# Kernel tuning notes

Hardware: AMD Instinct MI355X
Metric: run time of the kernel (lower is better)

The kernel has to match this reference:

```python
import jax, jax.numpy as jnp
import numpy as np

N_NODES = 50000

def mpnn_layer(x, edge_index, edge_weight, Wm, Wu, bu):
    # x: [N, Din]; Wm, Wu: [Dout, Din]; bu: [Dout]
    src, dst = edge_index[0], edge_index[1]
    m = x @ Wm.T                                   # [N, Dout] linear message
    msg = edge_weight[:, None] * m[src]            # gather + weight  [E, Dout]
    agg = jax.ops.segment_sum(msg, dst, num_segments=N_NODES)  # scatter-add
    return jnp.tanh(x @ Wu.T + bu + agg)

def setup_inputs() -> dict:
    key = jax.random.key(0)
    ks = jax.random.split(key, 16)
    N, E, D_IN, H, OUT = N_NODES, 800000, 128, 128, 32
    inp = {
        'x': jax.random.normal(ks[0], (N, D_IN), dtype=jnp.float32),
        'edge_index': jax.random.randint(ks[1], (2, E), 0, N, dtype=jnp.int64),
        'edge_weight': jax.random.uniform(ks[2], (E,), dtype=jnp.float32),
    }
    scale = 0.05
    dims = [D_IN, H, H]  # per-layer input dims
    for l in range(3):
        inp[f'Wm{l}'] = jax.random.normal(ks[3 + 3 * l], (H, dims[l]), dtype=jnp.float32) * scale
        inp[f'Wu{l}'] = jax.random.normal(ks[4 + 3 * l], (H, dims[l]), dtype=jnp.float32) * scale
        inp[f'bu{l}'] = jnp.zeros((H,), dtype=jnp.float32)
    inp['Wout'] = jax.random.normal(ks[13], (OUT, H), dtype=jnp.float32) * scale
    inp['bout'] = jnp.zeros((OUT,), dtype=jnp.float32)
    return inp

def reference(x, edge_index, edge_weight, Wm0, Wu0, bu0, Wm1, Wu1, bu1, Wm2, Wu2, bu2, Wout, bout):
    h = x
    for Wm, Wu, bu in ((Wm0, Wu0, bu0), (Wm1, Wu1, bu1), (Wm2, Wu2, bu2)):
        h = mpnn_layer(h, edge_index, edge_weight, Wm, Wu, bu)
    return h @ Wout.T + bout
```

## Files before the change

kernel.cpp:

```cpp
#include <hip/hip_runtime.h>
#include <hip/hip_bf16.h>
#include <cstddef>


typedef __attribute__((ext_vector_type(8))) short short8;
typedef __attribute__((ext_vector_type(4))) float f32x4;
typedef unsigned short ushort_t;
typedef unsigned int uint_t;

#define BSH 8
#define BSZ 256
#define CAPB 6144
#define TSTRIDE 16
#define EPB 2048

__device__ inline ushort_t f2bf(float f) {
    uint_t u = __float_as_uint(f);
    uint_t r = u + 0x7FFFu + ((u >> 16) & 1u);
    return (ushort_t)(r >> 16);
}
__device__ inline float bf_lo(uint_t u) { return __uint_as_float(u << 16); }
__device__ inline float bf_hi(uint_t u) { return __uint_as_float(u & 0xFFFF0000u); }
__device__ inline uint_t packbf(float a, float b) {
    return (uint_t)f2bf(a) | ((uint_t)f2bf(b) << 16);
}

__device__ inline float fast_tanh(float x) {
    float e = __builtin_amdgcn_exp2f(x * 2.8853900817779268f);
    return 1.f - 2.f * __builtin_amdgcn_rcpf(e + 1.f);
}

__device__ inline int get_dst(const int* __restrict__ ei, int e, int E, int f) {
    if (f) return ei[E + e];
    return ((const int2*)ei)[(size_t)E + e].x;
}
__device__ inline int get_src(const int* __restrict__ ei, int e, int E, int f) {
    if (f) return ei[e];
    return ((const int2*)ei)[e].x;
}

struct SetupArgs {
    const float* Wm0; const float* Wu0;
    const float* Wm1; const float* Wu1;
    const float* Wm2; const float* Wu2;
    const float* Wout;
    const float* x; const int* ei;
    ushort_t* wswz;
    ushort_t* woswz;
    ushort_t* xb;
    int* tails;
    int* flag;
    int N, E, TI;
    int ZT, WB, XB;
};
__global__ __launch_bounds__(256) void setup_kernel(SetupArgs a) {
    int bx = blockIdx.x, t = threadIdx.x;
    if (bx < a.ZT) {
        int i = bx * 256 + t;
        if (i < a.TI) a.tails[i] = 0;
        return;
    }
    bx -= a.ZT;
    if (bx == 0) {
        __shared__ int any;
        if (t == 0) any = 0;
        __syncthreads();
        int n = a.E < 2048 ? a.E : 2048;
        for (int i = t; i < n; i += 256)
            if (a.ei[2 * i + 1] != 0) any = 1;
        __syncthreads();
        if (t == 0) a.flag[0] = any;
        return;
    }
    bx -= 1;
    if (bx < a.WB) {
        int i = bx * 256 + t;
        if (i < 3 * 32768) {
            int l = i >> 15, r2 = i & 32767;
            int ct = r2 >> 12, ks = (r2 >> 9) & 7, lane = (r2 >> 3) & 63, j = r2 & 7;
            int col = ct * 16 + (lane & 15);
            int k = ks * 32 + (lane >> 4) * 8 + j;
            const float* Wm = l == 0 ? a.Wm0 : (l == 1 ? a.Wm1 : a.Wm2);
            const float* Wu = l == 0 ? a.Wu0 : (l == 1 ? a.Wu1 : a.Wu2);
            float v = k < 128 ? Wm[col * 128 + k] : Wu[col * 128 + (k - 128)];
            a.wswz[(size_t)l * 32768 + r2] = f2bf(v);
        } else if (i < 3 * 32768 + 4096) {
            int r2 = i - 3 * 32768;
            int ct = r2 >> 11, ks = (r2 >> 9) & 3, lane = (r2 >> 3) & 63, j = r2 & 7;
            int col = ct * 16 + (lane & 15);
            int k = ks * 32 + (lane >> 4) * 8 + j;
            a.woswz[r2] = f2bf(a.Wout[col * 128 + k]);
        }
        return;
    }
    bx -= a.WB;
    {
        int j = bx * 256 + t;
        if (j < a.N * 32) {
            float4 v = *(const float4*)(a.x + (size_t)j * 4);
            uint2 o;
            o.x = packbf(v.x, v.y);
            o.y = packbf(v.z, v.w);
            *(uint2*)(a.xb + (size_t)j * 4) = o;
        }
    }
}

__global__ __launch_bounds__(256) void bin_kernel(
    const int* __restrict__ ei, const float* __restrict__ ew,
    const int* __restrict__ flag, int* __restrict__ tails,
    uint2* __restrict__ staged, int E, int NB) {
    __shared__ uint2 ent[EPB];
    __shared__ int cnt[256], cur[256], runbase[256];
    const int tid = threadIdx.x;
    const int e0 = blockIdx.x * EPB;
    const int nE = (E - e0) < EPB ? (E - e0) : EPB;
    const int f = flag[0];
    cnt[tid] = 0;
    cur[tid] = 0;
    __syncthreads();
    for (int i = tid; i < nE; i += 256) {
        int e = e0 + i;
        int s = get_src(ei, e, E, f);
        int d = get_dst(ei, e, E, f);
        uint2 v;
        v.x = (uint_t)s | ((uint_t)f2bf(ew[e]) << 16);
        v.y = (uint_t)d;
        ent[i] = v;
        atomicAdd(&cnt[d >> BSH], 1);
    }
    __syncthreads();
    if (tid < NB) {
        int c = cnt[tid];
        runbase[tid] = c ? atomicAdd(&tails[tid * TSTRIDE], c) : 0;
    }
    __syncthreads();
    for (int i = tid; i < nE; i += 256) {
        uint2 v = ent[i];
        int d = (int)v.y;
        int b = d >> BSH;
        int lp = atomicAdd(&cur[b], 1);
        int gp = runbase[b] + lp;
        if (gp < CAPB) {
            uint2 o;
            o.x = v.x;
            o.y = (uint_t)(d & (BSZ - 1));
            staged[(size_t)b * CAPB + gp] = o;
        }
    }
}

__global__ __launch_bounds__(256) void place_kernel(
    const uint2* __restrict__ staged, const int* __restrict__ tails,
    int* __restrict__ cursor, uint_t* __restrict__ csr,
    int2* __restrict__ rowdeg, int N) {
    __shared__ int cnt[256], cur[256], excl[256], sm[256];
    __shared__ int baseSh;
    __shared__ uint_t outb[CAPB];
    const int b = blockIdx.x, tid = threadIdx.x;
    const int node0 = b << BSH;
    int tot = tails[b * TSTRIDE];
    tot = tot < CAPB ? tot : CAPB;
    cnt[tid] = 0;
    __syncthreads();
    const uint2* sp = staged + ((size_t)b * CAPB);
    for (int i = tid; i < tot; i += 256) atomicAdd(&cnt[sp[i].y], 1);
    __syncthreads();
    int c0 = cnt[tid];
    sm[tid] = c0;
    __syncthreads();
    for (int o = 1; o < 256; o <<= 1) {
        int v = tid >= o ? sm[tid - o] : 0;
        __syncthreads();
        sm[tid] += v;
        __syncthreads();
    }
    if (tid == 255) baseSh = atomicAdd(cursor, sm[255]);
    excl[tid] = sm[tid] - c0;
    cur[tid] = 0;
    __syncthreads();
    const int base = baseSh;
    for (int i = tid; i < tot; i += 256) {
        uint2 e = sp[i];
        int pos = excl[e.y] + atomicAdd(&cur[e.y], 1);
        outb[pos] = e.x;
    }
    __syncthreads();
    for (int i = tid; i < tot; i += 256) csr[base + i] = outb[i];
    if (node0 + tid < N) {
        int2 be;
        be.x = base + excl[tid];
        be.y = base + excl[tid] + c0;
        rowdeg[node0 + tid] = be;
    }
}

template <int WITH_OUT>
__global__ __launch_bounds__(512) void fused_layer(
    const uint_t* __restrict__ csr, const int2* __restrict__ rowdeg,
    const ushort_t* __restrict__ h, const ushort_t* __restrict__ Wswz,
    const float* __restrict__ bias, ushort_t* __restrict__ Hout,
    const ushort_t* __restrict__ Woswz, const float* __restrict__ bout,
    float* __restrict__ Cout, int N) {
    __shared__ ushort_t Gt[32 * 128];
    __shared__ ushort_t Ht[32 * 128];
    const int tid = threadIdx.x;
    const int lane = tid & 63;
    const int wv = tid >> 6;
    const int R0 = blockIdx.x * 32;
    const int slot = lane >> 3, f8 = lane & 7;

    const int pp = tid * 16;
    const int srow = pp >> 8;
    const int sx = (pp & 255) ^ ((srow & 7) << 4);
    uint4 hst = *(const uint4*)(h + (size_t)(R0 + srow) * 128 + (sx >> 1));

    int2 be[4];
#pragma unroll
    for (int i = 0; i < 4; ++i) {
        int nd = R0 + wv * 4 + i;
        if (nd < N) be[i] = rowdeg[nd];
        else { be[i].x = 0; be[i].y = 0; }
    }
#pragma unroll
    for (int i = 0; i < 4; ++i) {
        const int lr = wv * 4 + i;
        float s[16];
#pragma unroll
        for (int k = 0; k < 16; ++k) s[k] = 0.f;
        int j = be[i].x + slot;
        const int end = be[i].y;
        for (; j + 8 < end; j += 16) {
            uint_t p0 = csr[j];
            uint_t p1 = csr[j + 8];
            float w0 = bf_hi(p0), w1 = bf_hi(p1);
            const ushort_t* r0 = h + (size_t)(p0 & 0xFFFFu) * 128 + f8 * 16;
            const ushort_t* r1 = h + (size_t)(p1 & 0xFFFFu) * 128 + f8 * 16;
            uint4 v0 = *(const uint4*)(r0);
            uint4 v1 = *(const uint4*)(r0 + 8);
            uint4 u0 = *(const uint4*)(r1);
            uint4 u1 = *(const uint4*)(r1 + 8);
            s[0] += w0 * bf_lo(v0.x);  s[1] += w0 * bf_hi(v0.x);
            s[2] += w0 * bf_lo(v0.y);  s[3] += w0 * bf_hi(v0.y);
            s[4] += w0 * bf_lo(v0.z);  s[5] += w0 * bf_hi(v0.z);
            s[6] += w0 * bf_lo(v0.w);  s[7] += w0 * bf_hi(v0.w);
            s[8] += w0 * bf_lo(v1.x);  s[9] += w0 * bf_hi(v1.x);
            s[10] += w0 * bf_lo(v1.y); s[11] += w0 * bf_hi(v1.y);
            s[12] += w0 * bf_lo(v1.z); s[13] += w0 * bf_hi(v1.z);
            s[14] += w0 * bf_lo(v1.w); s[15] += w0 * bf_hi(v1.w);
            s[0] += w1 * bf_lo(u0.x);  s[1] += w1 * bf_hi(u0.x);
            s[2] += w1 * bf_lo(u0.y);  s[3] += w1 * bf_hi(u0.y);
            s[4] += w1 * bf_lo(u0.z);  s[5] += w1 * bf_hi(u0.z);
            s[6] += w1 * bf_lo(u0.w);  s[7] += w1 * bf_hi(u0.w);
            s[8] += w1 * bf_lo(u1.x);  s[9] += w1 * bf_hi(u1.x);
            s[10] += w1 * bf_lo(u1.y); s[11] += w1 * bf_hi(u1.y);
            s[12] += w1 * bf_lo(u1.z); s[13] += w1 * bf_hi(u1.z);
            s[14] += w1 * bf_lo(u1.w); s[15] += w1 * bf_hi(u1.w);
        }
        if (j < end) {
            uint_t p = csr[j];
            float w = bf_hi(p);
            const ushort_t* row = h + (size_t)(p & 0xFFFFu) * 128 + f8 * 16;
            uint4 v0 = *(const uint4*)(row);
            uint4 v1 = *(const uint4*)(row + 8);
            s[0] += w * bf_lo(v0.x);  s[1] += w * bf_hi(v0.x);
            s[2] += w * bf_lo(v0.y);  s[3] += w * bf_hi(v0.y);
            s[4] += w * bf_lo(v0.z);  s[5] += w * bf_hi(v0.z);
            s[6] += w * bf_lo(v0.w);  s[7] += w * bf_hi(v0.w);
            s[8] += w * bf_lo(v1.x);  s[9] += w * bf_hi(v1.x);
            s[10] += w * bf_lo(v1.y); s[11] += w * bf_hi(v1.y);
            s[12] += w * bf_lo(v1.z); s[13] += w * bf_hi(v1.z);
            s[14] += w * bf_lo(v1.w); s[15] += w * bf_hi(v1.w);
        }
#pragma unroll
        for (int k = 0; k < 16; ++k) s[k] += __shfl_xor(s[k], 8, 64);
#pragma unroll
        for (int k = 0; k < 16; ++k) s[k] += __shfl_xor(s[k], 16, 64);
#pragma unroll
        for (int k = 0; k < 16; ++k) s[k] += __shfl_xor(s[k], 32, 64);
        if (slot == 0) {
            uint4 o0, o1;
            o0.x = packbf(s[0], s[1]);   o0.y = packbf(s[2], s[3]);
            o0.z = packbf(s[4], s[5]);   o0.w = packbf(s[6], s[7]);
            o1.x = packbf(s[8], s[9]);   o1.y = packbf(s[10], s[11]);
            o1.z = packbf(s[12], s[13]); o1.w = packbf(s[14], s[15]);
            const int sw = (lr & 7) << 3;
            *(uint4*)(Gt + lr * 128 + ((f8 * 16) ^ sw)) = o0;
            *(uint4*)(Gt + lr * 128 + ((f8 * 16 + 8) ^ sw)) = o1;
        }
    }
    *(uint4*)((char*)Ht + pp) = hst;
    __syncthreads();

    const int gblk = wv & 1, ctp = wv >> 1;
    const int m = lane & 15, kg = lane >> 4;
    const int lrow = gblk * 16 + m;
    const int lsw = (lrow & 7) << 3;
    const int colL = lane & 15, rq = lane >> 4;

    short8 b0[8], b1[8];
#pragma unroll
    for (int ksp = 0; ksp < 8; ++ksp) {
        b0[ksp] = *(const short8*)(Wswz + (((2 * ctp) * 8 + ksp) * 64 + lane) * 8);
        b1[ksp] = *(const short8*)(Wswz + (((2 * ctp + 1) * 8 + ksp) * 64 + lane) * 8);
    }
    const float bv0 = bias[(2 * ctp) * 16 + colL];
    const float bv1 = bias[(2 * ctp + 1) * 16 + colL];

    f32x4 acc0 = (f32x4){0.f, 0.f, 0.f, 0.f};
    f32x4 acc1 = (f32x4){0.f, 0.f, 0.f, 0.f};
#pragma unroll
    for (int ksp = 0; ksp < 8; ++ksp) {
        const ushort_t* tp = (ksp < 4) ? Gt : Ht;
        short8 av = *(const short8*)(tp + lrow * 128 + (((ksp & 3) * 32 + kg * 8) ^ lsw));
        acc0 = __builtin_amdgcn_mfma_f32_16x16x32_bf16(av, b0[ksp], acc0, 0, 0, 0);
        acc1 = __builtin_amdgcn_mfma_f32_16x16x32_bf16(av, b1[ksp], acc1, 0, 0, 0);
    }
    float v0[4], v1[4];
#pragma unroll
    for (int reg = 0; reg < 4; ++reg) {
        v0[reg] = fast_tanh(acc0[reg] + bv0);
        v1[reg] = fast_tanh(acc1[reg] + bv1);
    }

    if (WITH_OUT == 0) {
#pragma unroll
        for (int reg = 0; reg < 4; ++reg) {
            int gr = R0 + gblk * 16 + rq * 4 + reg;
            if (gr < N) {
                Hout[(size_t)gr * 128 + (2 * ctp) * 16 + colL] = f2bf(v0[reg]);
                Hout[(size_t)gr * 128 + (2 * ctp + 1) * 16 + colL] = f2bf(v1[reg]);
            }
        }
    } else {
        __syncthreads();
#pragma unroll
        for (int reg = 0; reg < 4; ++reg) {
            int lr3 = gblk * 16 + rq * 4 + reg;
            int sw3 = (lr3 & 7) << 3;
            Gt[lr3 * 128 + (((2 * ctp) * 16 + colL) ^ sw3)] = f2bf(v0[reg]);
            Gt[lr3 * 128 + (((2 * ctp + 1) * 16 + colL) ^ sw3)] = f2bf(v1[reg]);
        }
        __syncthreads();
        if (wv < 4) {
            const int og = wv & 1, oc = wv >> 1;
            const int orow = og * 16 + m;
            const int osw = (orow & 7) << 3;
            short8 ob[4];
#pragma unroll
            for (int ks = 0; ks < 4; ++ks)
                ob[ks] = *(const short8*)(Woswz + ((oc * 4 + ks) * 64 + lane) * 8);
            f32x4 oacc = (f32x4){0.f, 0.f, 0.f, 0.f};
#pragma unroll
            for (int ks = 0; ks < 4; ++ks) {
                short8 av = *(const short8*)(Gt + orow * 128 + ((ks * 32 + kg * 8) ^ osw));
                oacc = __builtin_amdgcn_mfma_f32_16x16x32_bf16(av, ob[ks], oacc, 0, 0, 0);
            }
            const float obv = bout[oc * 16 + colL];
#pragma unroll
            for (int reg = 0; reg < 4; ++reg) {
                int gr = R0 + og * 16 + rq * 4 + reg;
                if (gr < N) Cout[(size_t)gr * 32 + oc * 16 + colL] = oacc[reg] + obv;
            }
        }
    }
}

extern "C" void kernel_launch(void* const* d_in, const int* in_sizes, int n_in,
                              void* d_out, int out_size, void* d_ws, size_t ws_size,
                              hipStream_t stream) {
    const float* x   = (const float*)d_in[0];
    const int* ei    = (const int*)d_in[1];
    const float* ew  = (const float*)d_in[2];
    const float* Wm[3] = {(const float*)d_in[3], (const float*)d_in[6], (const float*)d_in[9]};
    const float* Wu[3] = {(const float*)d_in[4], (const float*)d_in[7], (const float*)d_in[10]};
    const float* bu[3] = {(const float*)d_in[5], (const float*)d_in[8], (const float*)d_in[11]};
    const float* Wout = (const float*)d_in[12];
    const float* bout = (const float*)d_in[13];
    float* out = (float*)d_out;

    const int N = in_sizes[0] / 128;
    const int E = in_sizes[2];
    const size_t NPAD = 50048;
    const int NB = (N + BSZ - 1) / BSZ;
    const int TI = NB * TSTRIDE + 16;

    ushort_t* xb    = (ushort_t*)d_ws;
    ushort_t* hA    = xb + NPAD * 128;
    ushort_t* hB    = hA + NPAD * 128;
    ushort_t* gbuf  = hB + NPAD * 128;
    ushort_t* wswz  = gbuf + NPAD * 128;
    ushort_t* woswz = wswz + 3 * 32768;
    int* flag       = (int*)(woswz + 4096);
    int* tails      = flag + 1;
    int* cursor     = tails + NB * TSTRIDE;
    int* endp       = tails + TI;
    int2* rowdeg    = (int2*)(((uintptr_t)endp + 7) & ~(uintptr_t)7);
    uint2* staged   = (uint2*)(rowdeg + N + 8);
    uint_t* csr     = (uint_t*)(staged + (size_t)NB * CAPB);
    (void)ws_size;

    const int ZT = (TI + 255) / 256;
    const int WB = (3 * 32768 + 4096 + 255) / 256;
    const int XB = (N * 32 + 255) / 256;
    const int gB = (E + EPB - 1) / EPB;
    const int gF = (N + 31) / 32;

    SetupArgs sa;
    sa.Wm0 = Wm[0]; sa.Wu0 = Wu[0];
    sa.Wm1 = Wm[1]; sa.Wu1 = Wu[1];
    sa.Wm2 = Wm[2]; sa.Wu2 = Wu[2];
    sa.Wout = Wout; sa.x = x; sa.ei = ei;
    sa.wswz = wswz; sa.woswz = woswz; sa.xb = xb;
    sa.tails = tails; sa.flag = flag;
    sa.N = N; sa.E = E; sa.TI = TI;
    sa.ZT = ZT; sa.WB = WB; sa.XB = XB;
    setup_kernel<<<ZT + 1 + WB + XB, 256, 0, stream>>>(sa);

    bin_kernel<<<gB, 256, 0, stream>>>(ei, ew, flag, tails, staged, E, NB);
    place_kernel<<<NB, 256, 0, stream>>>(staged, tails, cursor, csr, rowdeg, N);

    fused_layer<0><<<gF, 512, 0, stream>>>(csr, rowdeg, xb, wswz, bu[0], hA,
                                           nullptr, nullptr, nullptr, N);
    fused_layer<0><<<gF, 512, 0, stream>>>(csr, rowdeg, hA, wswz + 32768, bu[1], hB,
                                           nullptr, nullptr, nullptr, N);
    fused_layer<1><<<gF, 512, 0, stream>>>(csr, rowdeg, hB, wswz + 2 * 32768, bu[2],
                                           nullptr, woswz, bout, out, N);
}
```

Before: 292.0 us.

## Sort binned edges locally, shrink fused layer tiles, deepen gather unroll

The bin kernel now does a shared-memory prefix scan and locally sorts each block's edges by bucket, so writes to the staged buffer become contiguous runs per bucket instead of scattered. The fused layer moves from 32-row, 512-thread blocks to 16-row, 256-thread blocks with launch bounds allowing four blocks per CU, which remaps each wave's MFMA output columns. The edge gather loop now issues four neighbour rows per iteration instead of two, using clamped indices and zero weights for the tail. The goal is more memory-level parallelism and occupancy in the gather-bound layers, at the cost of redundant clamped loads on short rows and extra LDS and scan work in binning.

```diff
diff --git a/kernel.cpp b/kernel.cpp
--- a/kernel.cpp
+++ b/kernel.cpp
@@ -111,7 +111,8 @@
     const int* __restrict__ flag, int* __restrict__ tails,
     uint2* __restrict__ staged, int E, int NB) {
     __shared__ uint2 ent[EPB];
-    __shared__ int cnt[256], cur[256], runbase[256];
+    __shared__ uint2 srt[EPB];
+    __shared__ int cnt[256], cur[256], exc[256], runbase[256];
     const int tid = threadIdx.x;
     const int e0 = blockIdx.x * EPB;
     const int nE = (E - e0) < EPB ? (E - e0) : EPB;
@@ -130,6 +131,15 @@
         atomicAdd(&cnt[d >> BSH], 1);
     }
     __syncthreads();
+    exc[tid] = cnt[tid];
+    __syncthreads();
+    for (int o = 1; o < 256; o <<= 1) {
+        int v = tid >= o ? exc[tid - o] : 0;
+        __syncthreads();
+        exc[tid] += v;
+        __syncthreads();
+    }
+    exc[tid] -= cnt[tid];
     if (tid < NB) {
         int c = cnt[tid];
         runbase[tid] = c ? atomicAdd(&tails[tid * TSTRIDE], c) : 0;
@@ -137,14 +147,19 @@
     __syncthreads();
     for (int i = tid; i < nE; i += 256) {
         uint2 v = ent[i];
-        int d = (int)v.y;
-        int b = d >> BSH;
+        int b = (int)(v.y >> BSH);
         int lp = atomicAdd(&cur[b], 1);
-        int gp = runbase[b] + lp;
+        srt[exc[b] + lp] = v;
+    }
+    __syncthreads();
+    for (int i = tid; i < nE; i += 256) {
+        uint2 v = srt[i];
+        int b = (int)(v.y >> BSH);
+        int gp = runbase[b] + (i - exc[b]);
         if (gp < CAPB) {
             uint2 o;
             o.x = v.x;
-            o.y = (uint_t)(d & (BSZ - 1));
+            o.y = (uint_t)(v.y & (BSZ - 1));
             staged[(size_t)b * CAPB + gp] = o;
         }
     }
@@ -195,19 +210,31 @@
     }
 }
 
+#define ACC16(W, V0, V1)                                         \
+    do {                                                         \
+        s[0] += (W) * bf_lo((V0).x);  s[1] += (W) * bf_hi((V0).x);  \
+        s[2] += (W) * bf_lo((V0).y);  s[3] += (W) * bf_hi((V0).y);  \
+        s[4] += (W) * bf_lo((V0).z);  s[5] += (W) * bf_hi((V0).z);  \
+        s[6] += (W) * bf_lo((V0).w);  s[7] += (W) * bf_hi((V0).w);  \
+        s[8] += (W) * bf_lo((V1).x);  s[9] += (W) * bf_hi((V1).x);  \
+        s[10] += (W) * bf_lo((V1).y); s[11] += (W) * bf_hi((V1).y); \
+        s[12] += (W) * bf_lo((V1).z); s[13] += (W) * bf_hi((V1).z); \
+        s[14] += (W) * bf_lo((V1).w); s[15] += (W) * bf_hi((V1).w); \
+    } while (0)
+
 template <int WITH_OUT>
-__global__ __launch_bounds__(512) void fused_layer(
+__global__ __launch_bounds__(256, 4) void fused_layer(
     const uint_t* __restrict__ csr, const int2* __restrict__ rowdeg,
     const ushort_t* __restrict__ h, const ushort_t* __restrict__ Wswz,
     const float* __restrict__ bias, ushort_t* __restrict__ Hout,
     const ushort_t* __restrict__ Woswz, const float* __restrict__ bout,
     float* __restrict__ Cout, int N) {
-    __shared__ ushort_t Gt[32 * 128];
-    __shared__ ushort_t Ht[32 * 128];
+    __shared__ ushort_t Gt[16 * 128];
+    __shared__ ushort_t Ht[16 * 128];
     const int tid = threadIdx.x;
     const int lane = tid & 63;
     const int wv = tid >> 6;
-    const int R0 = blockIdx.x * 32;
+    const int R0 = blockIdx.x * 16;
     const int slot = lane >> 3, f8 = lane & 7;
 
     const int pp = tid * 16;
@@ -215,62 +242,44 @@
     const int sx = (pp & 255) ^ ((srow & 7) << 4);
     uint4 hst = *(const uint4*)(h + (size_t)(R0 + srow) * 128 + (sx >> 1));
 
-    int2 be[4];
-#pragma unroll
-    for (int i = 0; i < 4; ++i) {
-        int nd = R0 + wv * 4 + i;
-        if (nd < N) be[i] = rowdeg[nd];
-        else { be[i].x = 0; be[i].y = 0; }
-    }
 #pragma unroll
     for (int i = 0; i < 4; ++i) {
         const int lr = wv * 4 + i;
+        const int nd = R0 + lr;
+        int beg = 0, end = 0;
+        if (nd < N) { int2 be = rowdeg[nd]; beg = be.x; end = be.y; }
         float s[16];
 #pragma unroll
         for (int k = 0; k < 16; ++k) s[k] = 0.f;
-        int j = be[i].x + slot;
-        const int end = be[i].y;
-        for (; j + 8 < end; j += 16) {
+        for (int j = beg + slot; j < end; j += 32) {
+            const int last = end - 1;
+            const int j1 = (j + 8) < last ? (j + 8) : last;
+            const int j2 = (j + 16) < last ? (j + 16) : last;
+            const int j3 = (j + 24) < last ? (j + 24) : last;
             uint_t p0 = csr[j];
-            uint_t p1 = csr[j + 8];
-            float w0 = bf_hi(p0), w1 = bf_hi(p1);
+            uint_t p1 = csr[j1];
+            uint_t p2 = csr[j2];
+            uint_t p3 = csr[j3];
             const ushort_t* r0 = h + (size_t)(p0 & 0xFFFFu) * 128 + f8 * 16;
             const ushort_t* r1 = h + (size_t)(p1 & 0xFFFFu) * 128 + f8 * 16;
-            uint4 v0 = *(const uint4*)(r0);
-            uint4 v1 = *(const uint4*)(r0 + 8);
-            uint4 u0 = *(const uint4*)(r1);
-            uint4 u1 = *(const uint4*)(r1 + 8);
-            s[0] += w0 * bf_lo(v0.x);  s[1] += w0 * bf_hi(v0.x);
-            s[2] += w0 * bf_lo(v0.y);  s[3] += w0 * bf_hi(v0.y);
-            s[4] += w0 * bf_lo(v0.z);  s[5] += w0 * bf_hi(v0.z);
-            s[6] += w0 * bf_lo(v0.w);  s[7] += w0 * bf_hi(v0.w);
-            s[8] += w0 * bf_lo(v1.x);  s[9] += w0 * bf_hi(v1.x);
-            s[10] += w0 * bf_lo(v1.y); s[11] += w0 * bf_hi(v1.y);
-            s[12] += w0 * bf_lo(v1.z); s[13] += w0 * bf_hi(v1.z);
-            s[14] += w0 * bf_lo(v1.w); s[15] += w0 * bf_hi(v1.w);
-            s[0] += w1 * bf_lo(u0.x);  s[1] += w1 * bf_hi(u0.x);
-            s[2] += w1 * bf_lo(u0.y);  s[3] += w1 * bf_hi(u0.y);
-            s[4] += w1 * bf_lo(u0.z);  s[5] += w1 * bf_hi(u0.z);
-            s[6] += w1 * bf_lo(u0.w);  s[7] += w1 * bf_hi(u0.w);
-            s[8] += w1 * bf_lo(u1.x);  s[9] += w1 * bf_hi(u1.x);
-            s[10] += w1 * bf_lo(u1.y); s[11] += w1 * bf_hi(u1.y);
-            s[12] += w1 * bf_lo(u1.z); s[13] += w1 * bf_hi(u1.z);
-            s[14] += w1 * bf_lo(u1.w); s[15] += w1 * bf_hi(u1.w);
-        }
-        if (j < end) {
-            uint_t p = csr[j];
-            float w = bf_hi(p);
-            const ushort_t* row = h + (size_t)(p & 0xFFFFu) * 128 + f8 * 16;
-            uint4 v0 = *(const uint4*)(row);
-            uint4 v1 = *(const uint4*)(row + 8);
-            s[0] += w * bf_lo(v0.x);  s[1] += w * bf_hi(v0.x);
-            s[2] += w * bf_lo(v0.y);  s[3] += w * bf_hi(v0.y);
-            s[4] += w * bf_lo(v0.z);  s[5] += w * bf_hi(v0.z);
-            s[6] += w * bf_lo(v0.w);  s[7] += w * bf_hi(v0.w);
-            s[8] += w * bf_lo(v1.x);  s[9] += w * bf_hi(v1.x);
-            s[10] += w * bf_lo(v1.y); s[11] += w * bf_hi(v1.y);
-            s[12] += w * bf_lo(v1.z); s[13] += w * bf_hi(v1.z);
-            s[14] += w * bf_lo(v1.w); s[15] += w * bf_hi(v1.w);
+            const ushort_t* r2 = h + (size_t)(p2 & 0xFFFFu) * 128 + f8 * 16;
+            const ushort_t* r3 = h + (size_t)(p3 & 0xFFFFu) * 128 + f8 * 16;
+            uint4 a0 = *(const uint4*)(r0);
+            uint4 a1 = *(const uint4*)(r0 + 8);
+            uint4 b0 = *(const uint4*)(r1);
+            uint4 b1 = *(const uint4*)(r1 + 8);
+            uint4 c0 = *(const uint4*)(r2);
+            uint4 c1 = *(const uint4*)(r2 + 8);
+            uint4 d0 = *(const uint4*)(r3);
+            uint4 d1 = *(const uint4*)(r3 + 8);
+            float w0 = bf_hi(p0);
+            float w1 = (j + 8) < end ? bf_hi(p1) : 0.f;
+            float w2 = (j + 16) < end ? bf_hi(p2) : 0.f;
+            float w3 = (j + 24) < end ? bf_hi(p3) : 0.f;
+            ACC16(w0, a0, a1);
+            ACC16(w1, b0, b1);
+            ACC16(w2, c0, c1);
+            ACC16(w3, d0, d1);
         }
 #pragma unroll
         for (int k = 0; k < 16; ++k) s[k] += __shfl_xor(s[k], 8, 64);
@@ -292,29 +301,27 @@
     *(uint4*)((char*)Ht + pp) = hst;
     __syncthreads();
 
-    const int gblk = wv & 1, ctp = wv >> 1;
     const int m = lane & 15, kg = lane >> 4;
-    const int lrow = gblk * 16 + m;
-    const int lsw = (lrow & 7) << 3;
+    const int lsw = (m & 7) << 3;
     const int colL = lane & 15, rq = lane >> 4;
 
-    short8 b0[8], b1[8];
+    short8 b0f[8], b1f[8];
 #pragma unroll
     for (int ksp = 0; ksp < 8; ++ksp) {
-        b0[ksp] = *(const short8*)(Wswz + (((2 * ctp) * 8 + ksp) * 64 + lane) * 8);
-        b1[ksp] = *(const short8*)(Wswz + (((2 * ctp + 1) * 8 + ksp) * 64 + lane) * 8);
-    }
-    const float bv0 = bias[(2 * ctp) * 16 + colL];
-    const float bv1 = bias[(2 * ctp + 1) * 16 + colL];
+        b0f[ksp] = *(const short8*)(Wswz + (((2 * wv) * 8 + ksp) * 64 + lane) * 8);
+        b1f[ksp] = *(const short8*)(Wswz + (((2 * wv + 1) * 8 + ksp) * 64 + lane) * 8);
+    }
+    const float bv0 = bias[(2 * wv) * 16 + colL];
+    const float bv1 = bias[(2 * wv + 1) * 16 + colL];
 
     f32x4 acc0 = (f32x4){0.f, 0.f, 0.f, 0.f};
     f32x4 acc1 = (f32x4){0.f, 0.f, 0.f, 0.f};
 #pragma unroll
     for (int ksp = 0; ksp < 8; ++ksp) {
         const ushort_t* tp = (ksp < 4) ? Gt : Ht;
-        short8 av = *(const short8*)(tp + lrow * 128 + (((ksp & 3) * 32 + kg * 8) ^ lsw));
-        acc0 = __builtin_amdgcn_mfma_f32_16x16x32_bf16(av, b0[ksp], acc0, 0, 0, 0);
-        acc1 = __builtin_amdgcn_mfma_f32_16x16x32_bf16(av, b1[ksp], acc1, 0, 0, 0);
+        short8 av = *(const short8*)(tp + m * 128 + (((ksp & 3) * 32 + kg * 8) ^ lsw));
+        acc0 = __builtin_amdgcn_mfma_f32_16x16x32_bf16(av, b0f[ksp], acc0, 0, 0, 0);
+        acc1 = __builtin_amdgcn_mfma_f32_16x16x32_bf16(av, b1f[ksp], acc1, 0, 0, 0);
     }
     float v0[4], v1[4];
 #pragma unroll
@@ -326,26 +333,25 @@
     if (WITH_OUT == 0) {
 #pragma unroll
         for (int reg = 0; reg < 4; ++reg) {
-            int gr = R0 + gblk * 16 + rq * 4 + reg;
+            int gr = R0 + rq * 4 + reg;
             if (gr < N) {
-                Hout[(size_t)gr * 128 + (2 * ctp) * 16 + colL] = f2bf(v0[reg]);
-                Hout[(size_t)gr * 128 + (2 * ctp + 1) * 16 + colL] = f2bf(v1[reg]);
+                Hout[(size_t)gr * 128 + (2 * wv) * 16 + colL] = f2bf(v0[reg]);
+                Hout[(size_t)gr * 128 + (2 * wv + 1) * 16 + colL] = f2bf(v1[reg]);
             }
         }
     } else {
         __syncthreads();
 #pragma unroll
         for (int reg = 0; reg < 4; ++reg) {
-            int lr3 = gblk * 16 + rq * 4 + reg;
+            int lr3 = rq * 4 + reg;
             int sw3 = (lr3 & 7) << 3;
-            Gt[lr3 * 128 + (((2 * ctp) * 16 + colL) ^ sw3)] = f2bf(v0[reg]);
-            Gt[lr3 * 128 + (((2 * ctp + 1) * 16 + colL) ^ sw3)] = f2bf(v1[reg]);
-        }
-        __syncthreads();
-        if (wv < 4) {
-            const int og = wv & 1, oc = wv >> 1;
-            const int orow = og * 16 + m;
-            const int osw = (orow & 7) << 3;
+            Gt[lr3 * 128 + (((2 * wv) * 16 + colL) ^ sw3)] = f2bf(v0[reg]);
+            Gt[lr3 * 128 + (((2 * wv + 1) * 16 + colL) ^ sw3)] = f2bf(v1[reg]);
+        }
+        __syncthreads();
+        if (wv < 2) {
+            const int oc = wv;
+            const int osw = (m & 7) << 3;
             short8 ob[4];
 #pragma unroll
             for (int ks = 0; ks < 4; ++ks)
@@ -353,13 +359,13 @@
             f32x4 oacc = (f32x4){0.f, 0.f, 0.f, 0.f};
 #pragma unroll
             for (int ks = 0; ks < 4; ++ks) {
-                short8 av = *(const short8*)(Gt + orow * 128 + ((ks * 32 + kg * 8) ^ osw));
+                short8 av = *(const short8*)(Gt + m * 128 + ((ks * 32 + kg * 8) ^ osw));
                 oacc = __builtin_amdgcn_mfma_f32_16x16x32_bf16(av, ob[ks], oacc, 0, 0, 0);
             }
             const float obv = bout[oc * 16 + colL];
 #pragma unroll
             for (int reg = 0; reg < 4; ++reg) {
-                int gr = R0 + og * 16 + rq * 4 + reg;
+                int gr = R0 + rq * 4 + reg;
                 if (gr < N) Cout[(size_t)gr * 32 + oc * 16 + colL] = oacc[reg] + obv;
             }
         }
@@ -404,7 +410,7 @@
     const int WB = (3 * 32768 + 4096 + 255) / 256;
     const int XB = (N * 32 + 255) / 256;
     const int gB = (E + EPB - 1) / EPB;
-    const int gF = (N + 31) / 32;
+    const int gF = (N + 15) / 16;
 
     SetupArgs sa;
     sa.Wm0 = Wm[0]; sa.Wu0 = Wu[0];
@@ -420,10 +426,10 @@
     bin_kernel<<<gB, 256, 0, stream>>>(ei, ew, flag, tails, staged, E, NB);
     place_kernel<<<NB, 256, 0, stream>>>(staged, tails, cursor, csr, rowdeg, N);
 
-    fused_layer<0><<<gF, 512, 0, stream>>>(csr, rowdeg, xb, wswz, bu[0], hA,
+    fused_layer<0><<<gF, 256, 0, stream>>>(csr, rowdeg, xb, wswz, bu[0], hA,
                                            nullptr, nullptr, nullptr, N);
-    fused_layer<0><<<gF, 512, 0, stream>>>(csr, rowdeg, hA, wswz + 32768, bu[1], hB,
+    fused_layer<0><<<gF, 256, 0, stream>>>(csr, rowdeg, hA, wswz + 32768, bu[1], hB,
                                            nullptr, nullptr, nullptr, N);
-    fused_layer<1><<<gF, 512, 0, stream>>>(csr, rowdeg, hB, wswz + 2 * 32768, bu[2],
+    fused_layer<1><<<gF, 256, 0, stream>>>(csr, rowdeg, hB, wswz + 2 * 32768, bu[2],
                                            nullptr, woswz, bout, out, N);
 }
```

After: 258.4 us. -11.5%, faster.
